# Optimization experiments

Hardware: AMD Instinct MI355X
Metric: run time of the kernel (lower is better)

## Reference

```python
import jax, jax.numpy as jnp
import numpy as np

B, T, J, D = 64, 2048, 128, 256

def setup_inputs() -> dict:
    key = jax.random.key(0)
    k1, k2, k3 = jax.random.split(key, 3)
    H = jax.random.normal(k1, (B, T, D), dtype=jnp.float32)
    U = jax.random.normal(k2, (B, J, D), dtype=jnp.float32)
    w = jax.random.normal(k3, (3 * D, 1), dtype=jnp.float32) * 0.05
    return {"H": H, "U": U, "w": w}


def reference(H, U, w):
    # Original: tile H to (B,T,J,D), tile U to (B,T,J,D), concat [H,U,H*U] -> (B,T,J,3D),
    # then dot with w (3D,1) and squeeze -> (B,T,J).
    # Equivalent trilinear form without materializing the tiled tensor:
    # S[b,t,j] = H[b,t]@w1 + U[b,j]@w2 + (H[b,t]*w3)@U[b,j]
    d = H.shape[-1]
    wv = w[:, 0]
    w1, w2, w3 = wv[:d], wv[d:2 * d], wv[2 * d:]
    s_h = jnp.einsum('btd,d->bt', H, w1)          # (B,T)
    s_u = jnp.einsum('bjd,d->bj', U, w2)          # (B,J)
    s_hu = jnp.einsum('btd,bjd->btj', H * w3, U)  # (B,T,J)
    return s_h[:, :, None] + s_u[:, None, :] + s_hu
```

## Files before the change

### kernel.cpp

```cpp
#include <hip/hip_runtime.h>
#include <stdint.h>

#define Bb 64
#define Tt 2048
#define Jj 128
#define Dd 256


typedef __attribute__((ext_vector_type(8))) __bf16 bf16x8;
typedef __attribute__((ext_vector_type(8))) unsigned short ushort8v;
typedef __attribute__((ext_vector_type(4))) float f32x4;

__device__ __forceinline__ unsigned short f2bf(float f) {
    unsigned int u = __builtin_bit_cast(unsigned int, f);
    u += 0x7FFFu + ((u >> 16) & 1u);
    return (unsigned short)(u >> 16);
}

__device__ __forceinline__ float dot8(const float4& a0, const float4& a1,
                                      const float4& b0, const float4& b1) {
    return a0.x * b0.x + a0.y * b0.y + a0.z * b0.z + a0.w * b0.w +
           a1.x * b1.x + a1.y * b1.y + a1.z * b1.z + a1.w * b1.w;
}

__device__ __forceinline__ bf16x8 pack8(const float4& a0, const float4& a1) {
    ushort8v s;
    s[0] = f2bf(a0.x); s[1] = f2bf(a0.y); s[2] = f2bf(a0.z); s[3] = f2bf(a0.w);
    s[4] = f2bf(a1.x); s[5] = f2bf(a1.y); s[6] = f2bf(a1.z); s[7] = f2bf(a1.w);
    return __builtin_bit_cast(bf16x8, s);
}

__device__ __forceinline__ bf16x8 pack8_scaled(const float4& a0, const float4& a1,
                                               const float4& s0, const float4& s1) {
    ushort8v s;
    s[0] = f2bf(a0.x * s0.x); s[1] = f2bf(a0.y * s0.y);
    s[2] = f2bf(a0.z * s0.z); s[3] = f2bf(a0.w * s0.w);
    s[4] = f2bf(a1.x * s1.x); s[5] = f2bf(a1.y * s1.y);
    s[6] = f2bf(a1.z * s1.z); s[7] = f2bf(a1.w * s1.w);
    return __builtin_bit_cast(bf16x8, s);
}

__global__ __launch_bounds__(256, 2)
void sim_kernel(const float* __restrict__ H, const float* __restrict__ U,
                const float* __restrict__ w, float* __restrict__ out) {
    const int tid   = threadIdx.x;
    const int wid   = tid >> 6;
    const int lane  = tid & 63;
    const int row16 = lane & 15;
    const int quad  = lane >> 4;

    const int b  = blockIdx.x >> 3;
    const int m0 = (blockIdx.x & 7) * 256 + wid * 64;

    const float* Hw = H + ((size_t)b * Tt + m0 + row16) * Dd + quad * 8;
    const float* Uw = U + ((size_t)b * Jj + row16) * Dd + quad * 8;
    const float* wq = w + quad * 8;

    f32x4 acc[4][8];
#pragma unroll
    for (int i = 0; i < 4; ++i)
#pragma unroll
        for (int j = 0; j < 8; ++j)
            acc[i][j] = (f32x4){0.f, 0.f, 0.f, 0.f};

    float sh[4] = {0.f, 0.f, 0.f, 0.f};
    float su[8] = {0.f, 0.f, 0.f, 0.f, 0.f, 0.f, 0.f, 0.f};

#pragma unroll 1
    for (int kb = 0; kb < Dd / 32; ++kb) {
        const int k0 = kb * 32;

        const float4 w1a = *(const float4*)(wq + k0);
        const float4 w1b = *(const float4*)(wq + k0 + 4);
        const float4 w2a = *(const float4*)(wq + Dd + k0);
        const float4 w2b = *(const float4*)(wq + Dd + k0 + 4);
        const float4 w3a = *(const float4*)(wq + 2 * Dd + k0);
        const float4 w3b = *(const float4*)(wq + 2 * Dd + k0 + 4);

        bf16x8 af[4];
#pragma unroll
        for (int i = 0; i < 4; ++i) {
            const float* hp = Hw + (size_t)i * 16 * Dd + k0;
            const float4 h0 = *(const float4*)(hp);
            const float4 h1 = *(const float4*)(hp + 4);
            sh[i] += dot8(h0, h1, w1a, w1b);
            af[i] = pack8_scaled(h0, h1, w3a, w3b);
        }

        bf16x8 bfr[8];
#pragma unroll
        for (int j = 0; j < 8; ++j) {
            const float* up = Uw + (size_t)j * 16 * Dd + k0;
            const float4 u0 = *(const float4*)(up);
            const float4 u1 = *(const float4*)(up + 4);
            su[j] += dot8(u0, u1, w2a, w2b);
            bfr[j] = pack8(u0, u1);
        }

#pragma unroll
        for (int i = 0; i < 4; ++i)
#pragma unroll
            for (int j = 0; j < 8; ++j)
                acc[i][j] = __builtin_amdgcn_mfma_f32_16x16x32_bf16(
                    af[i], bfr[j], acc[i][j], 0, 0, 0);
    }

#pragma unroll
    for (int i = 0; i < 4; ++i) {
        sh[i] += __shfl_xor(sh[i], 16);
        sh[i] += __shfl_xor(sh[i], 32);
    }
#pragma unroll
    for (int j = 0; j < 8; ++j) {
        su[j] += __shfl_xor(su[j], 16);
        su[j] += __shfl_xor(su[j], 32);
    }

    float* outW = out + ((size_t)b * Tt + m0) * Jj;
#pragma unroll
    for (int i = 0; i < 4; ++i) {
        float shv[4];
#pragma unroll
        for (int rg = 0; rg < 4; ++rg)
            shv[rg] = __shfl(sh[i], quad * 4 + rg);
#pragma unroll
        for (int j = 0; j < 8; ++j) {
            const int col = j * 16 + row16;
#pragma unroll
            for (int rg = 0; rg < 4; ++rg) {
                const int r = i * 16 + quad * 4 + rg;
                outW[(size_t)r * Jj + col] = acc[i][j][rg] + shv[rg] + su[j];
            }
        }
    }
}

extern "C" void kernel_launch(void* const* d_in, const int* in_sizes, int n_in,
                              void* d_out, int out_size, void* d_ws, size_t ws_size,
                              hipStream_t stream) {
    const float* H = (const float*)d_in[0];
    const float* U = (const float*)d_in[1];
    const float* w = (const float*)d_in[2];
    float* out = (float*)d_out;

    const int blocks = Bb * (Tt / 256);
    sim_kernel<<<blocks, 256, 0, stream>>>(H, U, w, out);
}
```

Before: 269.6 us.

## Precompute bf16 U fragments and U-bias in prep kernels, shrink main tile

```diff
diff --git a/kernel.cpp b/kernel.cpp
--- a/kernel.cpp
+++ b/kernel.cpp
@@ -30,108 +30,107 @@
     return __builtin_bit_cast(bf16x8, s);
 }
 
-__device__ __forceinline__ bf16x8 pack8_scaled(const float4& a0, const float4& a1,
-                                               const float4& s0, const float4& s1) {
+__global__ __launch_bounds__(256)
+void prep_u(const float* __restrict__ U, const float* __restrict__ w,
+            unsigned short* __restrict__ Up) {
+    const int idx = blockIdx.x * 256 + threadIdx.x;
+    const int b  = idx >> 12;
+    const int j  = (idx >> 9) & 7;
+    const int ks = (idx >> 6) & 7;
+    const int l  = idx & 63;
+    const int row = j * 16 + (l & 15);
+    const int k0  = ks * 32 + (l >> 4) * 8;
+
+    const float* up = U + ((size_t)(b * Jj + row)) * Dd + k0;
+    const float* wp = w + 2 * Dd + k0;
+    const float4 u0 = *(const float4*)(up);
+    const float4 u1 = *(const float4*)(up + 4);
+    const float4 w0 = *(const float4*)(wp);
+    const float4 w1 = *(const float4*)(wp + 4);
+
     ushort8v s;
-    s[0] = f2bf(a0.x * s0.x); s[1] = f2bf(a0.y * s0.y);
-    s[2] = f2bf(a0.z * s0.z); s[3] = f2bf(a0.w * s0.w);
-    s[4] = f2bf(a1.x * s1.x); s[5] = f2bf(a1.y * s1.y);
-    s[6] = f2bf(a1.z * s1.z); s[7] = f2bf(a1.w * s1.w);
-    return __builtin_bit_cast(bf16x8, s);
+    s[0] = f2bf(u0.x * w0.x); s[1] = f2bf(u0.y * w0.y);
+    s[2] = f2bf(u0.z * w0.z); s[3] = f2bf(u0.w * w0.w);
+    s[4] = f2bf(u1.x * w1.x); s[5] = f2bf(u1.y * w1.y);
+    s[6] = f2bf(u1.z * w1.z); s[7] = f2bf(u1.w * w1.w);
+    ((ushort8v*)Up)[idx] = s;
 }
 
-__global__ __launch_bounds__(256, 2)
-void sim_kernel(const float* __restrict__ H, const float* __restrict__ U,
-                const float* __restrict__ w, float* __restrict__ out) {
+__global__ __launch_bounds__(128)
+void prep_su(const float* __restrict__ U, const float* __restrict__ w,
+             float* __restrict__ su) {
+    const int b = blockIdx.x, col = threadIdx.x;
+    const float* up = U + ((size_t)b * Jj + col) * Dd;
+    const float* w2 = w + Dd;
+    float s = 0.f;
+#pragma unroll 4
+    for (int d = 0; d < Dd; d += 4) {
+        const float4 u = *(const float4*)(up + d);
+        const float4 v = *(const float4*)(w2 + d);
+        s += u.x * v.x + u.y * v.y + u.z * v.z + u.w * v.w;
+    }
+    su[b * Jj + col] = s;
+}
+
+__global__ __launch_bounds__(256, 4)
+void sim_main(const float* __restrict__ H, const unsigned short* __restrict__ Up,
+              const float* __restrict__ w, const float* __restrict__ su,
+              float* __restrict__ out) {
     const int tid   = threadIdx.x;
     const int wid   = tid >> 6;
     const int lane  = tid & 63;
     const int row16 = lane & 15;
     const int quad  = lane >> 4;
 
-    const int b  = blockIdx.x >> 3;
-    const int m0 = (blockIdx.x & 7) * 256 + wid * 64;
+    const int b  = blockIdx.x >> 5;
+    const int m0 = ((blockIdx.x & 31) * 4 + wid) * 16;
 
-    const float* Hw = H + ((size_t)b * Tt + m0 + row16) * Dd + quad * 8;
-    const float* Uw = U + ((size_t)b * Jj + row16) * Dd + quad * 8;
+    const float* Hp = H + ((size_t)(b * Tt + m0 + row16)) * Dd + quad * 8;
+    const unsigned short* Ub = Up + (size_t)b * 8 * 8 * 512;
     const float* wq = w + quad * 8;
 
-    f32x4 acc[4][8];
+    f32x4 acc[8];
 #pragma unroll
-    for (int i = 0; i < 4; ++i)
-#pragma unroll
-        for (int j = 0; j < 8; ++j)
-            acc[i][j] = (f32x4){0.f, 0.f, 0.f, 0.f};
-
-    float sh[4] = {0.f, 0.f, 0.f, 0.f};
-    float su[8] = {0.f, 0.f, 0.f, 0.f, 0.f, 0.f, 0.f, 0.f};
+    for (int j = 0; j < 8; ++j) acc[j] = (f32x4){0.f, 0.f, 0.f, 0.f};
+    float sh = 0.f;
 
 #pragma unroll 1
-    for (int kb = 0; kb < Dd / 32; ++kb) {
-        const int k0 = kb * 32;
-
-        const float4 w1a = *(const float4*)(wq + k0);
-        const float4 w1b = *(const float4*)(wq + k0 + 4);
-        const float4 w2a = *(const float4*)(wq + Dd + k0);
-        const float4 w2b = *(const float4*)(wq + Dd + k0 + 4);
-        const float4 w3a = *(const float4*)(wq + 2 * Dd + k0);
-        const float4 w3b = *(const float4*)(wq + 2 * Dd + k0 + 4);
-
-        bf16x8 af[4];
-#pragma unroll
-        for (int i = 0; i < 4; ++i) {
-            const float* hp = Hw + (size_t)i * 16 * Dd + k0;
-            const float4 h0 = *(const float4*)(hp);
-            const float4 h1 = *(const float4*)(hp + 4);
-            sh[i] += dot8(h0, h1, w1a, w1b);
-            af[i] = pack8_scaled(h0, h1, w3a, w3b);
-        }
+    for (int ks = 0; ks < 8; ++ks) {
+        const float4 h0 = *(const float4*)(Hp + ks * 32);
+        const float4 h1 = *(const float4*)(Hp + ks * 32 + 4);
 
         bf16x8 bfr[8];
 #pragma unroll
-        for (int j = 0; j < 8; ++j) {
-            const float* up = Uw + (size_t)j * 16 * Dd + k0;
-            const float4 u0 = *(const float4*)(up);
-            const float4 u1 = *(const float4*)(up + 4);
-            su[j] += dot8(u0, u1, w2a, w2b);
-            bfr[j] = pack8(u0, u1);
-        }
+        for (int j = 0; j < 8; ++j)
+            bfr[j] = __builtin_bit_cast(bf16x8,
+                *(const ushort8v*)(Ub + ((size_t)(j * 8 + ks) * 64 + lane) * 8));
 
+        const float4 w1a = *(const float4*)(wq + ks * 32);
+        const float4 w1b = *(const float4*)(wq + ks * 32 + 4);
+        sh += dot8(h0, h1, w1a, w1b);
+
+        const bf16x8 af = pack8(h0, h1);
 #pragma unroll
-        for (int i = 0; i < 4; ++i)
-#pragma unroll
-            for (int j = 0; j < 8; ++j)
-                acc[i][j] = __builtin_amdgcn_mfma_f32_16x16x32_bf16(
-                    af[i], bfr[j], acc[i][j], 0, 0, 0);
+        for (int j = 0; j < 8; ++j)
+            acc[j] = __builtin_amdgcn_mfma_f32_16x16x32_bf16(af, bfr[j], acc[j], 0, 0, 0);
     }
 
+    sh += __shfl_xor(sh, 16);
+    sh += __shfl_xor(sh, 32);
+    float shv[4];
 #pragma unroll
-    for (int i = 0; i < 4; ++i) {
-        sh[i] += __shfl_xor(sh[i], 16);
-        sh[i] += __shfl_xor(sh[i], 32);
-    }
+    for (int rg = 0; rg < 4; ++rg)
+        shv[rg] = __shfl(sh, quad * 4 + rg);
+
+    float* outW = out + ((size_t)(b * Tt + m0)) * Jj;
+    const float* sub = su + b * Jj;
 #pragma unroll
     for (int j = 0; j < 8; ++j) {
-        su[j] += __shfl_xor(su[j], 16);
-        su[j] += __shfl_xor(su[j], 32);
-    }
-
-    float* outW = out + ((size_t)b * Tt + m0) * Jj;
-#pragma unroll
-    for (int i = 0; i < 4; ++i) {
-        float shv[4];
+        const int col = j * 16 + row16;
+        const float suv = sub[col];
 #pragma unroll
         for (int rg = 0; rg < 4; ++rg)
-            shv[rg] = __shfl(sh[i], quad * 4 + rg);
-#pragma unroll
-        for (int j = 0; j < 8; ++j) {
-            const int col = j * 16 + row16;
-#pragma unroll
-            for (int rg = 0; rg < 4; ++rg) {
-                const int r = i * 16 + quad * 4 + rg;
-                outW[(size_t)r * Jj + col] = acc[i][j][rg] + shv[rg] + su[j];
-            }
-        }
+            outW[(size_t)(quad * 4 + rg) * Jj + col] = acc[j][rg] + shv[rg] + suv;
     }
 }
 
@@ -143,6 +142,10 @@
     const float* w = (const float*)d_in[2];
     float* out = (float*)d_out;
 
-    const int blocks = Bb * (Tt / 256);
-    sim_kernel<<<blocks, 256, 0, stream>>>(H, U, w, out);
+    unsigned short* Up = (unsigned short*)d_ws;
+    float* su = (float*)((char*)d_ws + (size_t)Bb * Jj * Dd * 2);
+
+    prep_u<<<1024, 256, 0, stream>>>(U, w, Up);
+    prep_su<<<Bb, 128, 0, stream>>>(U, w, su);
+    sim_main<<<Bb * 32, 256, 0, stream>>>(H, Up, w, su, out);
 }
```

After: 247.4 us. 8.2% less time.
